# Kernel optimization log

Measured on AMD Instinct MI355X. Metric: run time of the kernel, lower is better.

Reference implementation:

```python
import jax, jax.numpy as jnp
import numpy as np
import math

NUM_HEADS = 16
D_MODEL = 1024
B, T = 1, 4096


def setup_inputs() -> dict:
    key = jax.random.key(0)
    kx, kq, kk, kv, ko = jax.random.split(key, 5)
    s = 1.0 / math.sqrt(D_MODEL)
    return {
        "x": jax.random.normal(kx, (B, T, D_MODEL), dtype=jnp.float32),
        "Wq": jax.random.normal(kq, (D_MODEL, D_MODEL), dtype=jnp.float32) * s,
        "Wk": jax.random.normal(kk, (D_MODEL, D_MODEL), dtype=jnp.float32) * s,
        "Wv": jax.random.normal(kv, (D_MODEL, D_MODEL), dtype=jnp.float32) * s,
        "Wo": jax.random.normal(ko, (D_MODEL, D_MODEL), dtype=jnp.float32) * s,
    }


def reference(x, Wq, Wk, Wv, Wo):
    # x: (B, T, D); weights stored torch-Linear style: y = x @ W.T
    Bx, Tx, D = x.shape
    H = NUM_HEADS
    dk = D // H
    q = (x @ Wq.T).reshape(Bx, Tx, H, dk)  # (B,T,H,dk)
    k = (x @ Wk.T).reshape(Bx, Tx, H, dk)
    v = (x @ Wv.T).reshape(Bx, Tx, H, dk)
    # scores: (B,H,T,T), scaled dot-product
    scores = jnp.einsum("bthd,bshd->bhts", q, k) / math.sqrt(dk)
    causal_mask = jnp.triu(jnp.ones((Tx, Tx), dtype=bool), k=1)  # True above diag
    scores = jnp.where(causal_mask, jnp.float32(-jnp.inf), scores).astype(jnp.float32)
    attn = jax.nn.softmax(scores, axis=-1)  # fp32 softmax, as in the torch module
    out = jnp.einsum("bhts,bshd->bthd", attn, v).reshape(Bx, Tx, D)
    return out @ Wo.T
```

## Files before the change

### kernel.cpp

```cpp
#include <hip/hip_runtime.h>
#include <hip/hip_bf16.h>
#include <math.h>

typedef __attribute__((ext_vector_type(8)))  __bf16 bf16x8;
typedef __attribute__((ext_vector_type(4)))  __bf16 bf16x4;
typedef __attribute__((ext_vector_type(4)))  float  f32x4;
typedef __attribute__((ext_vector_type(16))) float  f32x16;

static constexpr int T_SEQ = 4096;
static constexpr int DM    = 1024;
static constexpr int NH    = 16;
static constexpr float QSCALE = 0.125f * 1.44269504088896340736f;

__device__ __forceinline__ void gload16(const void* g, void* l) {
    __builtin_amdgcn_global_load_lds(
        (const __attribute__((address_space(1))) unsigned int*)g,
        (__attribute__((address_space(3))) unsigned int*)l,
        16, 0, 0);
}

__device__ __forceinline__ unsigned cvtpk_bf16(float a, float b) {
    unsigned r;
    asm("v_cvt_pk_bf16_f32 %0, %1, %2" : "=v"(r) : "v"(a), "v"(b));
    return r;
}
__device__ __forceinline__ void permswap(unsigned& x, unsigned& y) {
    asm("v_permlane32_swap_b32 %0, %1" : "+v"(x), "+v"(y));
}

__global__ __launch_bounds__(256)
void cvt_bf16(const float* __restrict__ in, __bf16* __restrict__ out, int n4) {
    int i = blockIdx.x * blockDim.x + threadIdx.x;
    if (i >= n4) return;
    float4 v = ((const float4*)in)[i];
    bf16x4 o;
    o[0] = (__bf16)v.x; o[1] = (__bf16)v.y; o[2] = (__bf16)v.z; o[3] = (__bf16)v.w;
    ((bf16x4*)out)[i] = o;
}

__global__ __launch_bounds__(256)
void cvt4_bf16(const float* __restrict__ a0, const float* __restrict__ a1,
               const float* __restrict__ a2, const float* __restrict__ a3,
               __bf16* __restrict__ o0, __bf16* __restrict__ o1,
               __bf16* __restrict__ o2, __bf16* __restrict__ o3, int n4) {
    int i = blockIdx.x * blockDim.x + threadIdx.x;
    if (i >= n4) return;
    const float* in = blockIdx.y == 0 ? a0 : blockIdx.y == 1 ? a1 : blockIdx.y == 2 ? a2 : a3;
    __bf16* out     = blockIdx.y == 0 ? o0 : blockIdx.y == 1 ? o1 : blockIdx.y == 2 ? o2 : o3;
    float4 v = ((const float4*)in)[i];
    bf16x4 o;
    o[0] = (__bf16)v.x; o[1] = (__bf16)v.y; o[2] = (__bf16)v.z; o[3] = (__bf16)v.w;
    ((bf16x4*)out)[i] = o;
}

template<bool OUT_BF16>
__device__ __forceinline__ void gemm_body(const __bf16* __restrict__ A,
                                          const __bf16* __restrict__ B,
                                          void* __restrict__ Cout,
                                          int N, int K, float scale,
                                          int bx, int by) {
    __shared__ __align__(16) __bf16 Al[128 * 64];
    __shared__ __align__(16) __bf16 Bl[128 * 64];
    const int tid  = threadIdx.x;
    const int lane = tid & 63;
    const int wid  = tid >> 6;
    const int wr   = wid >> 1, wc = wid & 1;
    const int m0   = by * 128, n0 = bx * 128;
    const int r    = lane & 15, g = lane >> 4;

    f32x4 acc[4][4];
    const f32x4 z4 = {0.f, 0.f, 0.f, 0.f};
    #pragma unroll
    for (int i = 0; i < 4; ++i)
        #pragma unroll
        for (int j = 0; j < 4; ++j) acc[i][j] = z4;

    for (int kt = 0; kt < K; kt += 64) {
        __syncthreads();
        #pragma unroll
        for (int p = 0; p < 4; ++p) {
            int u    = p * 256 + tid;
            int row  = u >> 3;
            int col8 = (u & 7) ^ (row & 7);
            gload16(A + (size_t)(m0 + row) * K + kt + col8 * 8,
                    (char*)Al + (p * 256 + wid * 64) * 16);
            gload16(B + (size_t)(n0 + row) * K + kt + col8 * 8,
                    (char*)Bl + (p * 256 + wid * 64) * 16);
        }
        __syncthreads();
        __builtin_amdgcn_s_setprio(1);
        #pragma unroll
        for (int kk = 0; kk < 2; ++kk) {
            bf16x8 af[4], bfr[4];
            #pragma unroll
            for (int mi = 0; mi < 4; ++mi)
                af[mi] = *(const bf16x8*)&Al[(wr * 64 + mi * 16 + r) * 64 + (((kk * 4 + g) ^ (r & 7)) * 8)];
            #pragma unroll
            for (int nj = 0; nj < 4; ++nj)
                bfr[nj] = *(const bf16x8*)&Bl[(wc * 64 + nj * 16 + r) * 64 + (((kk * 4 + g) ^ (r & 7)) * 8)];
            #pragma unroll
            for (int mi = 0; mi < 4; ++mi)
                #pragma unroll
                for (int nj = 0; nj < 4; ++nj)
                    acc[mi][nj] = __builtin_amdgcn_mfma_f32_16x16x32_bf16(af[mi], bfr[nj], acc[mi][nj], 0, 0, 0);
        }
        __builtin_amdgcn_s_setprio(0);
    }
    #pragma unroll
    for (int mi = 0; mi < 4; ++mi)
        #pragma unroll
        for (int nj = 0; nj < 4; ++nj)
            #pragma unroll
            for (int j = 0; j < 4; ++j) {
                int row = m0 + wr * 64 + mi * 16 + g * 4 + j;
                int col = n0 + wc * 64 + nj * 16 + r;
                float v = acc[mi][nj][j] * scale;
                if (OUT_BF16) ((__bf16*)Cout)[(size_t)row * N + col] = (__bf16)v;
                else          ((float*)Cout)[(size_t)row * N + col]  = v;
            }
}

__global__ __launch_bounds__(256)
void gemm_qkv(const __bf16* __restrict__ A,
              const __bf16* __restrict__ W0, const __bf16* __restrict__ W1,
              const __bf16* __restrict__ W2,
              __bf16* __restrict__ O0, __bf16* __restrict__ O1, __bf16* __restrict__ O2) {
    const int z = blockIdx.z;
    const __bf16* B = z == 0 ? W0 : (z == 1 ? W1 : W2);
    __bf16*       C = z == 0 ? O0 : (z == 1 ? O1 : O2);
    float scale = z == 0 ? QSCALE : 1.0f;
    gemm_body<true>(A, B, C, DM, DM, scale, blockIdx.x, blockIdx.y);
}

__global__ __launch_bounds__(256)
void gemm_out(const __bf16* __restrict__ A, const __bf16* __restrict__ B,
              float* __restrict__ C) {
    gemm_body<false>(A, B, C, DM, DM, 1.0f, blockIdx.x, blockIdx.y);
}

__global__ __launch_bounds__(256)
void vtrans(const __bf16* __restrict__ V, __bf16* __restrict__ Vt) {
    __shared__ __bf16 tl[64][72];
    const int tid = threadIdx.x;
    const int t0  = blockIdx.x * 64;
    const int h   = blockIdx.y;
    #pragma unroll
    for (int p = 0; p < 2; ++p) {
        int c = p * 256 + tid, row = c >> 3, col8 = c & 7;
        *(bf16x8*)&tl[row][col8 * 8] =
            *(const bf16x8*)(V + (size_t)(t0 + row) * DM + h * 64 + col8 * 8);
    }
    __syncthreads();
    #pragma unroll
    for (int p = 0; p < 2; ++p) {
        int c = p * 256 + tid, d = c >> 3, tc8 = c & 7;
        bf16x8 o;
        #pragma unroll
        for (int e = 0; e < 8; ++e) o[e] = tl[tc8 * 8 + e][d];
        *(bf16x8*)(Vt + (size_t)(h * 64 + d) * T_SEQ + t0 + tc8 * 8) = o;
    }
}

__global__ __launch_bounds__(128)
void attn_fwd(const __bf16* __restrict__ Q, const __bf16* __restrict__ Kp,
              const __bf16* __restrict__ Vt, __bf16* __restrict__ O)
{
    __shared__ __align__(16) __bf16 Kl[2][64 * 64];
    __shared__ __align__(16) __bf16 Vl[2][64 * 64];
    const int tid  = threadIdx.x;
    const int lane = tid & 63, wid = tid >> 6;
    const int l31  = lane & 31;
    const int hi   = lane >> 5;
    const int h    = blockIdx.x;
    const int qb   = (T_SEQ / 64 - 1) - blockIdx.y;
    const int qw   = qb * 64 + wid * 32;
    const int qg   = qw + l31;

    bf16x8 qf[4];
    #pragma unroll
    for (int kd0 = 0; kd0 < 4; ++kd0)
        qf[kd0] = *(const bf16x8*)(Q + (size_t)qg * DM + h * 64 + kd0 * 16 + hi * 8);

    float m_i = -1e30f, l_i = 0.f;
    f32x16 oacc[2];
    #pragma unroll
    for (int d = 0; d < 2; ++d)
        #pragma unroll
        for (int e = 0; e < 16; ++e) oacc[d][e] = 0.f;

    const int nt = qb + 1;

    auto stage = [&](int t, int buf) {
        #pragma unroll
        for (int p = 0; p < 4; ++p) {
            int u    = p * 128 + tid;
            int row  = u >> 3;
            int col8 = (u & 7) ^ (row & 7);
            gload16(Kp + (size_t)(t * 64 + row) * DM + h * 64 + col8 * 8,
                    (char*)&Kl[buf][0] + (p * 128 + wid * 64) * 16);
            gload16(Vt + (size_t)(h * 64 + row) * T_SEQ + t * 64 + col8 * 8,
                    (char*)&Vl[buf][0] + (p * 128 + wid * 64) * 16);
        }
    };

    stage(0, 0);
    int cur = 0;
    for (int t = 0; t < nt; ++t) {
        __syncthreads();
        if (t + 1 < nt) stage(t + 1, cur ^ 1);
        f32x16 sf[2];
        #pragma unroll
        for (int ks = 0; ks < 2; ++ks)
            #pragma unroll
            for (int e = 0; e < 16; ++e) sf[ks][e] = 0.f;
        __builtin_amdgcn_s_setprio(1);
        #pragma unroll
        for (int ksub = 0; ksub < 2; ++ksub) {
            const int row = ksub * 32 + l31;
            #pragma unroll
            for (int kd0 = 0; kd0 < 4; ++kd0) {
                bf16x8 kf = *(const bf16x8*)
                    &Kl[cur][(row << 6) + ((((kd0 << 1) + hi) ^ (row & 7)) << 3)];
                sf[ksub] = __builtin_amdgcn_mfma_f32_32x32x16_bf16(kf, qf[kd0], sf[ksub], 0, 0, 0);
            }
        }
        __builtin_amdgcn_s_setprio(0);
        if (t == qb) {
            const int kb = (t << 6) + 4 * hi;
            #pragma unroll
            for (int ksub = 0; ksub < 2; ++ksub)
                #pragma unroll
                for (int e = 0; e < 16; ++e) {
                    int k = kb + ksub * 32 + ((e & 3) + 8 * (e >> 2));
                    if (k > qg) sf[ksub][e] = -1e30f;
                }
        }
        float pm;
        {
            float t0[8];
            #pragma unroll
            for (int e = 0; e < 8; ++e)
                t0[e] = fmaxf(fmaxf(sf[0][e], sf[0][e + 8]), fmaxf(sf[1][e], sf[1][e + 8]));
            #pragma unroll
            for (int s = 4; s > 0; s >>= 1)
                #pragma unroll
                for (int e = 0; e < s; ++e) t0[e] = fmaxf(t0[e], t0[e + s]);
            pm = t0[0];
        }
        pm = fmaxf(pm, __shfl_xor(pm, 32));
        if (pm > m_i + 8.f) {
            float al = exp2f(m_i - pm);
            m_i = pm;
            l_i *= al;
            #pragma unroll
            for (int d = 0; d < 2; ++d)
                #pragma unroll
                for (int e = 0; e < 16; ++e) oacc[d][e] *= al;
        }
        float p[32];
        #pragma unroll
        for (int i = 0; i < 32; ++i)
            p[i] = exp2f(sf[i >> 4][i & 15] - m_i);
        {
            float s0[8];
            #pragma unroll
            for (int e = 0; e < 8; ++e)
                s0[e] = (p[e] + p[e + 8]) + (p[e + 16] + p[e + 24]);
            #pragma unroll
            for (int s = 4; s > 0; s >>= 1)
                #pragma unroll
                for (int e = 0; e < s; ++e) s0[e] += s0[e + s];
            float rs = s0[0];
            rs += __shfl_xor(rs, 32);
            l_i += rs;
        }
        __builtin_amdgcn_s_setprio(1);
        #pragma unroll
        for (int ks = 0; ks < 4; ++ks) {
            unsigned w0 = cvtpk_bf16(p[8 * ks + 0], p[8 * ks + 1]);
            unsigned w1 = cvtpk_bf16(p[8 * ks + 2], p[8 * ks + 3]);
            unsigned w2 = cvtpk_bf16(p[8 * ks + 4], p[8 * ks + 5]);
            unsigned w3 = cvtpk_bf16(p[8 * ks + 6], p[8 * ks + 7]);
            permswap(w0, w2);
            permswap(w1, w3);
            union { unsigned u[4]; bf16x8 v; } pu;
            pu.u[0] = w0; pu.u[1] = w1; pu.u[2] = w2; pu.u[3] = w3;
            #pragma unroll
            for (int dsub = 0; dsub < 2; ++dsub) {
                const int row = dsub * 32 + l31;
                bf16x8 vt = *(const bf16x8*)
                    &Vl[cur][(row << 6) + ((((ks << 1) + hi) ^ (row & 7)) << 3)];
                oacc[dsub] = __builtin_amdgcn_mfma_f32_32x32x16_bf16(vt, pu.v, oacc[dsub], 0, 0, 0);
            }
        }
        __builtin_amdgcn_s_setprio(0);
        cur ^= 1;
    }
    __syncthreads();
    __bf16* ow = &Kl[0][0] + wid * 2048;
    const float invl = 1.f / l_i;
    #pragma unroll
    for (int dsub = 0; dsub < 2; ++dsub)
        #pragma unroll
        for (int e = 0; e < 16; ++e) {
            int d = dsub * 32 + ((e & 3) + 8 * (e >> 2)) + 4 * hi;
            float v = oacc[dsub][e] * invl;
            int bo = l31 * 128 + ((2 * d) ^ ((l31 & 7) << 4));
            *(__bf16*)((char*)ow + bo) = (__bf16)v;
        }
    #pragma unroll
    for (int i = 0; i < 4; ++i) {
        int u  = hi * 4 + i;
        int bo = l31 * 128 + ((u * 16) ^ ((l31 & 7) << 4));
        bf16x8 v8 = *(const bf16x8*)((char*)ow + bo);
        *(bf16x8*)(O + (size_t)qg * DM + h * 64 + u * 8) = v8;
    }
}

extern "C" void kernel_launch(void* const* d_in, const int* in_sizes, int n_in,
                              void* d_out, int out_size, void* d_ws, size_t ws_size,
                              hipStream_t stream) {
    const float* x  = (const float*)d_in[0];
    const float* Wq = (const float*)d_in[1];
    const float* Wk = (const float*)d_in[2];
    const float* Wv = (const float*)d_in[3];
    const float* Wo = (const float*)d_in[4];
    float* out = (float*)d_out;

    char* ws = (char*)d_ws;
    const size_t MB = (size_t)1 << 20;
    __bf16* xb    = (__bf16*)(ws + 0 * MB);
    __bf16* VtG   = (__bf16*)(ws + 0 * MB);
    __bf16* wqb   = (__bf16*)(ws + 8 * MB);
    __bf16* wkb   = (__bf16*)(ws + 10 * MB);
    __bf16* wvb   = (__bf16*)(ws + 12 * MB);
    __bf16* wob   = (__bf16*)(ws + 14 * MB);
    __bf16* Qb    = (__bf16*)(ws + 16 * MB);
    __bf16* Kb    = (__bf16*)(ws + 24 * MB);
    __bf16* Vb    = (__bf16*)(ws + 32 * MB);
    __bf16* attnb = (__bf16*)(ws + 40 * MB);

    const int nX = T_SEQ * DM / 4;
    const int nW = DM * DM / 4;
    cvt_bf16<<<(nX + 255) / 256, 256, 0, stream>>>(x, xb, nX);
    cvt4_bf16<<<dim3((nW + 255) / 256, 4), 256, 0, stream>>>(Wq, Wk, Wv, Wo,
                                                             wqb, wkb, wvb, wob, nW);

    gemm_qkv<<<dim3(DM / 128, T_SEQ / 128, 3), 256, 0, stream>>>(xb, wqb, wkb, wvb, Qb, Kb, Vb);

    vtrans<<<dim3(T_SEQ / 64, NH), 256, 0, stream>>>(Vb, VtG);

    attn_fwd<<<dim3(NH, T_SEQ / 64), 128, 0, stream>>>(Qb, Kb, VtG, attnb);

    gemm_out<<<dim3(DM / 128, T_SEQ / 128), 256, 0, stream>>>(attnb, wob, out);
}
```

Baseline: 190.6 us.

## Software-pipeline QK^T one tile ahead with register-staged K/V loads in attention

```diff
diff --git a/kernel.cpp b/kernel.cpp
--- a/kernel.cpp
+++ b/kernel.cpp
@@ -26,6 +26,20 @@
 }
 __device__ __forceinline__ void permswap(unsigned& x, unsigned& y) {
     asm("v_permlane32_swap_b32 %0, %1" : "+v"(x), "+v"(y));
+}
+__device__ __forceinline__ float xhalf_max(float v) {
+    union { float f; unsigned u; } a, b;
+    a.f = v; b.f = v;
+    asm volatile("" : "+v"(b.u));
+    permswap(a.u, b.u);
+    return fmaxf(a.f, b.f);
+}
+__device__ __forceinline__ float xhalf_sum(float v) {
+    union { float f; unsigned u; } a, b;
+    a.f = v; b.f = v;
+    asm volatile("" : "+v"(b.u));
+    permswap(a.u, b.u);
+    return a.f + b.f;
 }
 
 __global__ __launch_bounds__(256)
@@ -172,7 +186,8 @@
     const int l31  = lane & 31;
     const int hi   = lane >> 5;
     const int h    = blockIdx.x;
-    const int qb   = (T_SEQ / 64 - 1) - blockIdx.y;
+    const int u_   = blockIdx.y & 15, j_ = blockIdx.y >> 4;
+    const int qb   = j_ == 0 ? u_ : j_ == 1 ? 31 - u_ : j_ == 2 ? 32 + u_ : 63 - u_;
     const int qw   = qb * 64 + wid * 32;
     const int qg   = qw + l31;
 
@@ -190,7 +205,7 @@
 
     const int nt = qb + 1;
 
-    auto stage = [&](int t, int buf) {
+    auto stage_lds = [&](int t, int buf) {
         #pragma unroll
         for (int p = 0; p < 4; ++p) {
             int u    = p * 128 + tid;
@@ -202,39 +217,63 @@
                     (char*)&Vl[buf][0] + (p * 128 + wid * 64) * 16);
         }
     };
-
-    stage(0, 0);
-    int cur = 0;
-    for (int t = 0; t < nt; ++t) {
-        __syncthreads();
-        if (t + 1 < nt) stage(t + 1, cur ^ 1);
-        f32x16 sf[2];
-        #pragma unroll
-        for (int ks = 0; ks < 2; ++ks)
-            #pragma unroll
-            for (int e = 0; e < 16; ++e) sf[ks][e] = 0.f;
-        __builtin_amdgcn_s_setprio(1);
+    stage_lds(0, 0);
+    if (nt > 1) stage_lds(1, 1);
+    __syncthreads();
+
+    auto qk = [&](f32x16* sdst, int buf) {
         #pragma unroll
         for (int ksub = 0; ksub < 2; ++ksub) {
             const int row = ksub * 32 + l31;
+            f32x16 a;
+            #pragma unroll
+            for (int e = 0; e < 16; ++e) a[e] = 0.f;
             #pragma unroll
             for (int kd0 = 0; kd0 < 4; ++kd0) {
                 bf16x8 kf = *(const bf16x8*)
-                    &Kl[cur][(row << 6) + ((((kd0 << 1) + hi) ^ (row & 7)) << 3)];
-                sf[ksub] = __builtin_amdgcn_mfma_f32_32x32x16_bf16(kf, qf[kd0], sf[ksub], 0, 0, 0);
-            }
+                    &Kl[buf][(row << 6) + ((((kd0 << 1) + hi) ^ (row & 7)) << 3)];
+                a = __builtin_amdgcn_mfma_f32_32x32x16_bf16(kf, qf[kd0], a, 0, 0, 0);
+            }
+            sdst[ksub] = a;
+        }
+    };
+    auto mask_sf = [&](f32x16* s, int t) {
+        const int kb = (t << 6) + 4 * hi;
+        #pragma unroll
+        for (int ksub = 0; ksub < 2; ++ksub)
+            #pragma unroll
+            for (int e = 0; e < 16; ++e) {
+                int k = kb + ksub * 32 + ((e & 3) + 8 * (e >> 2));
+                if (k > qg) s[ksub][e] = -1e30f;
+            }
+    };
+
+    f32x16 sf[2], sfn[2];
+    qk(sf, 0);
+    if (qb == 0) mask_sf(sf, 0);
+
+    bf16x8 kreg[4], vreg[4];
+    for (int t = 0; t < nt; ++t) {
+        const int cur = t & 1;
+        const bool have_next  = (t + 1 < nt);
+        const bool have_next2 = (t + 2 < nt);
+        if (have_next2) {
+            const int t2 = t + 2;
+            #pragma unroll
+            for (int p = 0; p < 4; ++p) {
+                int u   = p * 128 + tid;
+                int row = u >> 3;
+                int c   = u & 7;
+                kreg[p] = *(const bf16x8*)(Kp + (size_t)(t2 * 64 + row) * DM + h * 64 + c * 8);
+                vreg[p] = *(const bf16x8*)(Vt + (size_t)(h * 64 + row) * T_SEQ + t2 * 64 + c * 8);
+            }
+        }
+        __builtin_amdgcn_s_setprio(1);
+        if (have_next) {
+            qk(sfn, cur ^ 1);
+            if (t + 1 == qb) mask_sf(sfn, t + 1);
         }
         __builtin_amdgcn_s_setprio(0);
-        if (t == qb) {
-            const int kb = (t << 6) + 4 * hi;
-            #pragma unroll
-            for (int ksub = 0; ksub < 2; ++ksub)
-                #pragma unroll
-                for (int e = 0; e < 16; ++e) {
-                    int k = kb + ksub * 32 + ((e & 3) + 8 * (e >> 2));
-                    if (k > qg) sf[ksub][e] = -1e30f;
-                }
-        }
         float pm;
         {
             float t0[8];
@@ -245,9 +284,8 @@
             for (int s = 4; s > 0; s >>= 1)
                 #pragma unroll
                 for (int e = 0; e < s; ++e) t0[e] = fmaxf(t0[e], t0[e + s]);
-            pm = t0[0];
-        }
-        pm = fmaxf(pm, __shfl_xor(pm, 32));
+            pm = xhalf_max(t0[0]);
+        }
         if (pm > m_i + 8.f) {
             float al = exp2f(m_i - pm);
             m_i = pm;
@@ -270,9 +308,7 @@
             for (int s = 4; s > 0; s >>= 1)
                 #pragma unroll
                 for (int e = 0; e < s; ++e) s0[e] += s0[e + s];
-            float rs = s0[0];
-            rs += __shfl_xor(rs, 32);
-            l_i += rs;
+            l_i += xhalf_sum(s0[0]);
         }
         __builtin_amdgcn_s_setprio(1);
         #pragma unroll
@@ -294,7 +330,22 @@
             }
         }
         __builtin_amdgcn_s_setprio(0);
-        cur ^= 1;
+        if (have_next2) {
+            __syncthreads();
+            #pragma unroll
+            for (int p = 0; p < 4; ++p) {
+                int u   = p * 128 + tid;
+                int row = u >> 3;
+                int c   = u & 7;
+                *(bf16x8*)&Kl[cur][(row << 6) + ((c ^ (row & 7)) << 3)] = kreg[p];
+                *(bf16x8*)&Vl[cur][(row << 6) + ((c ^ (row & 7)) << 3)] = vreg[p];
+            }
+            __syncthreads();
+        }
+        if (have_next) {
+            sf[0] = sfn[0];
+            sf[1] = sfn[1];
+        }
     }
     __syncthreads();
     __bf16* ow = &Kl[0][0] + wid * 2048;
@@ -350,7 +401,7 @@
 
     vtrans<<<dim3(T_SEQ / 64, NH), 256, 0, stream>>>(Vb, VtG);
 
-    attn_fwd<<<dim3(NH, T_SEQ / 64), 128, 0, stream>>>(Qb, Kb, VtG, attnb);
+    attn_fwd<<<dim3(NH, 64), 128, 0, stream>>>(Qb, Kb, VtG, attnb);
 
     gemm_out<<<dim3(DM / 128, T_SEQ / 128), 256, 0, stream>>>(attnb, wob, out);
 }
```

Measured after the change: 189.9 us. About the same (-0.4%).
